# Optimization experiments

Hardware: AMD Instinct MI355X
Metric: run time of the kernel (lower is better)

Reference implementation:

```python
import jax, jax.numpy as jnp
import numpy as np

N, D, T = 4096, 512, 4096
TEMPERATURE = 0.07
MARGIN = 0.5
CONT_WEIGHT = 1.0
TRIP_WEIGHT = 0.3
EPS = 1e-8        # eps in the log / denominator (matches torch code)
PD_EPS = 1e-6     # F.pairwise_distance default eps added to the difference


def setup_inputs() -> dict:
    key = jax.random.key(0)
    k1, k2, k3 = jax.random.split(key, 3)
    embeddings = jax.random.normal(k1, (N, D), dtype=jnp.float32)
    labels = jax.random.randint(k2, (N,), 0, 256)            # ~16 positives per place
    triplets = jax.random.randint(k3, (T, 3), 0, N)          # (anchor, pos, neg) indices
    return {"embeddings": embeddings, "labels": labels, "triplets": triplets}


def reference(embeddings, labels, triplets):
    # ---- MultiPositiveContrastiveLoss ----
    # F.cosine_similarity normalizes each row with eps=1e-8 on the norm.
    norms = jnp.linalg.norm(embeddings, axis=1, keepdims=True)
    n_emb = embeddings / jnp.maximum(norms, EPS)
    sim = (n_emb @ n_emb.T) / TEMPERATURE                    # [N, N]

    pos_mask = (labels[:, None] == labels[None, :]).astype(embeddings.dtype)
    pos_mask = pos_mask * (1.0 - jnp.eye(sim.shape[0], dtype=embeddings.dtype))

    exp_sim = jnp.exp(sim)
    pos_sum = (exp_sim * pos_mask).sum(axis=1)
    total_sum = exp_sim.sum(axis=1)
    loss = -jnp.log(pos_sum / (total_sum + EPS) + EPS)

    valid = pos_mask.sum(axis=1) > 0
    cnt = valid.sum()
    cont_loss = jnp.where(
        cnt > 0,
        jnp.where(valid, loss, 0.0).sum() / jnp.maximum(cnt, 1).astype(loss.dtype),
        jnp.zeros((), loss.dtype),
    )

    # ---- TripletLoss, vectorized over all triplets (replaces Python loop) ----
    a = embeddings[triplets[:, 0]]   # [T, D]
    p = embeddings[triplets[:, 1]]
    ng = embeddings[triplets[:, 2]]
    pos_dist = jnp.linalg.norm(a - p + PD_EPS, axis=1)
    neg_dist = jnp.linalg.norm(a - ng + PD_EPS, axis=1)
    trip_loss = jnp.maximum(pos_dist - neg_dist + MARGIN, 0.0).mean()

    total = CONT_WEIGHT * cont_loss + TRIP_WEIGHT * trip_loss
    return (total, cont_loss, trip_loss)
```

## Files before the change

### kernel.cpp

```cpp
#include <hip/hip_runtime.h>

#define NN 4096
#define DD 512
#define TT 4096

typedef __bf16 bf16x8 __attribute__((ext_vector_type(8)));
typedef float f32x4 __attribute__((ext_vector_type(4)));

constexpr float INV_TEMP = 1.0f / 0.07f;

#define AS1(p) ((__attribute__((address_space(1))) const void*)(p))
#define AS3(p) ((__attribute__((address_space(3))) void*)(p))

__global__ __launch_bounds__(256) void k_normalize(const float* __restrict__ emb,
                                                   __bf16* __restrict__ nemb) {
    int wave = threadIdx.x >> 6, lane = threadIdx.x & 63;
    int row = blockIdx.x * 4 + wave;
    const float4* src = (const float4*)(emb + (size_t)row * DD);
    float4 x0 = src[lane * 2 + 0];
    float4 x1 = src[lane * 2 + 1];
    float ss = x0.x * x0.x + x0.y * x0.y + x0.z * x0.z + x0.w * x0.w +
               x1.x * x1.x + x1.y * x1.y + x1.z * x1.z + x1.w * x1.w;
    #pragma unroll
    for (int m = 1; m < 64; m <<= 1) ss += __shfl_xor(ss, m, 64);
    float inv = 1.0f / fmaxf(sqrtf(ss), 1e-8f);
    bf16x8 v;
    v[0] = (__bf16)(x0.x * inv); v[1] = (__bf16)(x0.y * inv);
    v[2] = (__bf16)(x0.z * inv); v[3] = (__bf16)(x0.w * inv);
    v[4] = (__bf16)(x1.x * inv); v[5] = (__bf16)(x1.y * inv);
    v[6] = (__bf16)(x1.z * inv); v[7] = (__bf16)(x1.w * inv);
    *(bf16x8*)(nemb + (size_t)row * DD + lane * 8) = v;
}

__global__ __launch_bounds__(256) void k_contrast(const __bf16* __restrict__ nemb,
                                                  const int* __restrict__ labels,
                                                  float* __restrict__ posP,
                                                  float* __restrict__ totP,
                                                  float* __restrict__ cntP) {
    __shared__ __attribute__((aligned(16))) __bf16 aSm[128 * 32];
    __shared__ __attribute__((aligned(16))) __bf16 bSm[128 * 32];
    __shared__ int rlab[128];
    __shared__ int clab[128];

    int tid = threadIdx.x;
    int lane = tid & 63, wave = tid >> 6;
    int wr = wave >> 1, wc = wave & 1;
    int l15 = lane & 15, quad = lane >> 4;
    int rowblk = blockIdx.y, colblk = blockIdx.x;
    int row0 = rowblk * 128, col0 = colblk * 128;

    if (tid < 128) rlab[tid] = labels[row0 + tid];
    else           clab[tid - 128] = labels[col0 + tid - 128];

    f32x4 acc[4][4];
    #pragma unroll
    for (int r = 0; r < 4; ++r)
        #pragma unroll
        for (int c = 0; c < 4; ++c) {
            f32x4 z = {0.0f, 0.0f, 0.0f, 0.0f};
            acc[r][c] = z;
        }

    const __bf16* gA = nemb + (size_t)(row0 + (tid >> 2)) * DD + (tid & 3) * 8;
    const __bf16* gB = nemb + (size_t)(col0 + (tid >> 2)) * DD + (tid & 3) * 8;

    for (int kt = 0; kt < 16; ++kt) {
        int kb = kt * 32;
        __syncthreads();
        __builtin_amdgcn_global_load_lds(AS1(gA + kb),                     AS3(aSm + tid * 8),         16, 0, 0);
        __builtin_amdgcn_global_load_lds(AS1(gA + (size_t)64 * DD + kb),   AS3(aSm + (tid + 256) * 8), 16, 0, 0);
        __builtin_amdgcn_global_load_lds(AS1(gB + kb),                     AS3(bSm + tid * 8),         16, 0, 0);
        __builtin_amdgcn_global_load_lds(AS1(gB + (size_t)64 * DD + kb),   AS3(bSm + (tid + 256) * 8), 16, 0, 0);
        __syncthreads();

        bf16x8 af[4], bfr[4];
        #pragma unroll
        for (int r = 0; r < 4; ++r)
            af[r] = *(const bf16x8*)(aSm + (wr * 64 + r * 16 + l15) * 32 + quad * 8);
        #pragma unroll
        for (int c = 0; c < 4; ++c)
            bfr[c] = *(const bf16x8*)(bSm + (wc * 64 + c * 16 + l15) * 32 + quad * 8);
        #pragma unroll
        for (int r = 0; r < 4; ++r)
            #pragma unroll
            for (int c = 0; c < 4; ++c)
                acc[r][c] = __builtin_amdgcn_mfma_f32_16x16x32_bf16(af[r], bfr[c], acc[r][c], 0, 0, 0);
    }

    int cl[4];
    #pragma unroll
    for (int c = 0; c < 4; ++c) cl[c] = clab[wc * 64 + c * 16 + l15];

    #pragma unroll
    for (int r = 0; r < 4; ++r) {
        float tv[4] = {0, 0, 0, 0}, pv[4] = {0, 0, 0, 0}, cv[4] = {0, 0, 0, 0};
        int gibase = row0 + wr * 64 + r * 16 + quad * 4;
        int rl[4];
        #pragma unroll
        for (int v = 0; v < 4; ++v) rl[v] = rlab[wr * 64 + r * 16 + quad * 4 + v];
        #pragma unroll
        for (int c = 0; c < 4; ++c) {
            int gj = col0 + wc * 64 + c * 16 + l15;
            #pragma unroll
            for (int v = 0; v < 4; ++v) {
                float e = __expf(acc[r][c][v] * INV_TEMP);
                tv[v] += e;
                bool match = (rl[v] == cl[c]) && ((gibase + v) != gj);
                pv[v] += match ? e : 0.0f;
                cv[v] += match ? 1.0f : 0.0f;
            }
        }
        #pragma unroll
        for (int m = 1; m < 16; m <<= 1) {
            #pragma unroll
            for (int v = 0; v < 4; ++v) {
                tv[v] += __shfl_xor(tv[v], m, 64);
                pv[v] += __shfl_xor(pv[v], m, 64);
                cv[v] += __shfl_xor(cv[v], m, 64);
            }
        }
        if (l15 == 0) {
            #pragma unroll
            for (int v = 0; v < 4; ++v) {
                int gr = gibase + v;
                int oidx = gr * 64 + colblk * 2 + wc;
                posP[oidx] = pv[v];
                totP[oidx] = tv[v];
                cntP[oidx] = cv[v];
            }
        }
    }
}

__global__ __launch_bounds__(256) void k_triplet(const float* __restrict__ emb,
                                                 const int* __restrict__ trip,
                                                 float* __restrict__ tl) {
    int wave = threadIdx.x >> 6, lane = threadIdx.x & 63;
    int t = blockIdx.x * 4 + wave;
    int ia = trip[t * 3 + 0], ip = trip[t * 3 + 1], ig = trip[t * 3 + 2];
    const float4* pa = (const float4*)(emb + (size_t)ia * DD);
    const float4* pp = (const float4*)(emb + (size_t)ip * DD);
    const float4* pn = (const float4*)(emb + (size_t)ig * DD);
    float d1 = 0.0f, d2 = 0.0f;
    #pragma unroll
    for (int j = 0; j < 2; ++j) {
        float4 a = pa[lane * 2 + j];
        float4 p = pp[lane * 2 + j];
        float4 n = pn[lane * 2 + j];
        float dx;
        dx = a.x - p.x + 1e-6f; d1 += dx * dx;
        dx = a.y - p.y + 1e-6f; d1 += dx * dx;
        dx = a.z - p.z + 1e-6f; d1 += dx * dx;
        dx = a.w - p.w + 1e-6f; d1 += dx * dx;
        dx = a.x - n.x + 1e-6f; d2 += dx * dx;
        dx = a.y - n.y + 1e-6f; d2 += dx * dx;
        dx = a.z - n.z + 1e-6f; d2 += dx * dx;
        dx = a.w - n.w + 1e-6f; d2 += dx * dx;
    }
    #pragma unroll
    for (int m = 1; m < 64; m <<= 1) {
        d1 += __shfl_xor(d1, m, 64);
        d2 += __shfl_xor(d2, m, 64);
    }
    if (lane == 0) tl[t] = fmaxf(sqrtf(d1) - sqrtf(d2) + 0.5f, 0.0f);
}

__global__ __launch_bounds__(256) void k_rowloss(const float* __restrict__ posP,
                                                 const float* __restrict__ totP,
                                                 const float* __restrict__ cntP,
                                                 float* __restrict__ rloss,
                                                 float* __restrict__ rvalid) {
    int wave = threadIdx.x >> 6, lane = threadIdx.x & 63;
    int row = blockIdx.x * 4 + wave;
    float p = posP[row * 64 + lane];
    float t = totP[row * 64 + lane];
    float c = cntP[row * 64 + lane];
    #pragma unroll
    for (int m = 1; m < 64; m <<= 1) {
        p += __shfl_xor(p, m, 64);
        t += __shfl_xor(t, m, 64);
        c += __shfl_xor(c, m, 64);
    }
    if (lane == 0) {
        float loss = -logf(p / (t + 1e-8f) + 1e-8f);
        bool valid = c > 0.0f;
        rloss[row] = valid ? loss : 0.0f;
        rvalid[row] = valid ? 1.0f : 0.0f;
    }
}

__global__ __launch_bounds__(256) void k_final(const float* __restrict__ rloss,
                                               const float* __restrict__ rvalid,
                                               const float* __restrict__ tl,
                                               float* __restrict__ out) {
    int tid = threadIdx.x;
    float sl = 0.0f, sv = 0.0f, st = 0.0f;
    for (int i = tid; i < NN; i += 256) {
        sl += rloss[i];
        sv += rvalid[i];
        st += tl[i];
    }
    #pragma unroll
    for (int m = 1; m < 64; m <<= 1) {
        sl += __shfl_xor(sl, m, 64);
        sv += __shfl_xor(sv, m, 64);
        st += __shfl_xor(st, m, 64);
    }
    __shared__ float red[3][4];
    int lane = tid & 63, wave = tid >> 6;
    if (lane == 0) { red[0][wave] = sl; red[1][wave] = sv; red[2][wave] = st; }
    __syncthreads();
    if (tid == 0) {
        float SL = red[0][0] + red[0][1] + red[0][2] + red[0][3];
        float SV = red[1][0] + red[1][1] + red[1][2] + red[1][3];
        float ST = red[2][0] + red[2][1] + red[2][2] + red[2][3];
        float cont = (SV > 0.0f) ? (SL / SV) : 0.0f;
        float trip = ST * (1.0f / (float)TT);
        out[0] = cont + 0.3f * trip;
        out[1] = cont;
        out[2] = trip;
    }
}

extern "C" void kernel_launch(void* const* d_in, const int* in_sizes, int n_in,
                              void* d_out, int out_size, void* d_ws, size_t ws_size,
                              hipStream_t stream) {
    const float* emb = (const float*)d_in[0];
    const int* labels = (const int*)d_in[1];
    const int* trips = (const int*)d_in[2];
    float* out = (float*)d_out;
    char* ws = (char*)d_ws;

    __bf16* nemb  = (__bf16*)(ws);
    float* posP   = (float*)(ws + 4194304);
    float* totP   = (float*)(ws + 5242880);
    float* cntP   = (float*)(ws + 6291456);
    float* rloss  = (float*)(ws + 7340032);
    float* rvalid = (float*)(ws + 7356416);
    float* tl     = (float*)(ws + 7372800);

    k_normalize<<<NN / 4, 256, 0, stream>>>(emb, nemb);
    k_contrast<<<dim3(32, 32), 256, 0, stream>>>(nemb, labels, posP, totP, cntP);
    k_triplet<<<TT / 4, 256, 0, stream>>>(emb, trips, tl);
    k_rowloss<<<NN / 4, 256, 0, stream>>>(posP, totP, cntP, rloss, rvalid);
    k_final<<<1, 256, 0, stream>>>(rloss, rvalid, tl, out);
}
```

Measured before the change: 111.9 us.

## Exploit Gram matrix symmetry with triangular tiles and fuse normalize with triplet kernel

The contrastive kernel now computes only upper-triangular 128x128 block pairs of the symmetric similarity matrix. Each block is split into two 64-row halves, and each off-diagonal tile emits both row and column partial sums, so the N^2 MFMA and exp work is roughly halved. The normalize and triplet kernels are merged into one launch to save a launch and let them overlap. The cost is a smaller per-block tile with less operand reuse, extra column-direction reductions and stores, and a wider partial-sum buffer for the row-loss kernel to read.

```diff
diff --git a/kernel.cpp b/kernel.cpp
--- a/kernel.cpp
+++ b/kernel.cpp
@@ -12,24 +12,56 @@
 #define AS1(p) ((__attribute__((address_space(1))) const void*)(p))
 #define AS3(p) ((__attribute__((address_space(3))) void*)(p))
 
-__global__ __launch_bounds__(256) void k_normalize(const float* __restrict__ emb,
-                                                   __bf16* __restrict__ nemb) {
+__global__ __launch_bounds__(256) void k_normtrip(const float* __restrict__ emb,
+                                                  const int* __restrict__ trip,
+                                                  __bf16* __restrict__ nemb,
+                                                  float* __restrict__ tl) {
     int wave = threadIdx.x >> 6, lane = threadIdx.x & 63;
-    int row = blockIdx.x * 4 + wave;
-    const float4* src = (const float4*)(emb + (size_t)row * DD);
-    float4 x0 = src[lane * 2 + 0];
-    float4 x1 = src[lane * 2 + 1];
-    float ss = x0.x * x0.x + x0.y * x0.y + x0.z * x0.z + x0.w * x0.w +
-               x1.x * x1.x + x1.y * x1.y + x1.z * x1.z + x1.w * x1.w;
-    #pragma unroll
-    for (int m = 1; m < 64; m <<= 1) ss += __shfl_xor(ss, m, 64);
-    float inv = 1.0f / fmaxf(sqrtf(ss), 1e-8f);
-    bf16x8 v;
-    v[0] = (__bf16)(x0.x * inv); v[1] = (__bf16)(x0.y * inv);
-    v[2] = (__bf16)(x0.z * inv); v[3] = (__bf16)(x0.w * inv);
-    v[4] = (__bf16)(x1.x * inv); v[5] = (__bf16)(x1.y * inv);
-    v[6] = (__bf16)(x1.z * inv); v[7] = (__bf16)(x1.w * inv);
-    *(bf16x8*)(nemb + (size_t)row * DD + lane * 8) = v;
+    if (blockIdx.x < NN / 4) {
+        int row = blockIdx.x * 4 + wave;
+        const float4* src = (const float4*)(emb + (size_t)row * DD);
+        float4 x0 = src[lane * 2 + 0];
+        float4 x1 = src[lane * 2 + 1];
+        float ss = x0.x * x0.x + x0.y * x0.y + x0.z * x0.z + x0.w * x0.w +
+                   x1.x * x1.x + x1.y * x1.y + x1.z * x1.z + x1.w * x1.w;
+        #pragma unroll
+        for (int m = 1; m < 64; m <<= 1) ss += __shfl_xor(ss, m, 64);
+        float inv = 1.0f / fmaxf(sqrtf(ss), 1e-8f);
+        bf16x8 v;
+        v[0] = (__bf16)(x0.x * inv); v[1] = (__bf16)(x0.y * inv);
+        v[2] = (__bf16)(x0.z * inv); v[3] = (__bf16)(x0.w * inv);
+        v[4] = (__bf16)(x1.x * inv); v[5] = (__bf16)(x1.y * inv);
+        v[6] = (__bf16)(x1.z * inv); v[7] = (__bf16)(x1.w * inv);
+        *(bf16x8*)(nemb + (size_t)row * DD + lane * 8) = v;
+    } else {
+        int t = (blockIdx.x - NN / 4) * 4 + wave;
+        int ia = trip[t * 3 + 0], ip = trip[t * 3 + 1], ig = trip[t * 3 + 2];
+        const float4* pa = (const float4*)(emb + (size_t)ia * DD);
+        const float4* pp = (const float4*)(emb + (size_t)ip * DD);
+        const float4* pn = (const float4*)(emb + (size_t)ig * DD);
+        float d1 = 0.0f, d2 = 0.0f;
+        #pragma unroll
+        for (int j = 0; j < 2; ++j) {
+            float4 a = pa[lane * 2 + j];
+            float4 p = pp[lane * 2 + j];
+            float4 n = pn[lane * 2 + j];
+            float dx;
+            dx = a.x - p.x + 1e-6f; d1 += dx * dx;
+            dx = a.y - p.y + 1e-6f; d1 += dx * dx;
+            dx = a.z - p.z + 1e-6f; d1 += dx * dx;
+            dx = a.w - p.w + 1e-6f; d1 += dx * dx;
+            dx = a.x - n.x + 1e-6f; d2 += dx * dx;
+            dx = a.y - n.y + 1e-6f; d2 += dx * dx;
+            dx = a.z - n.z + 1e-6f; d2 += dx * dx;
+            dx = a.w - n.w + 1e-6f; d2 += dx * dx;
+        }
+        #pragma unroll
+        for (int m = 1; m < 64; m <<= 1) {
+            d1 += __shfl_xor(d1, m, 64);
+            d2 += __shfl_xor(d2, m, 64);
+        }
+        if (lane == 0) tl[t] = fmaxf(sqrtf(d1) - sqrtf(d2) + 0.5f, 0.0f);
+    }
 }
 
 __global__ __launch_bounds__(256) void k_contrast(const __bf16* __restrict__ nemb,
@@ -37,26 +69,34 @@
                                                   float* __restrict__ posP,
                                                   float* __restrict__ totP,
                                                   float* __restrict__ cntP) {
-    __shared__ __attribute__((aligned(16))) __bf16 aSm[128 * 32];
+    __shared__ __attribute__((aligned(16))) __bf16 aSm[64 * 32];
     __shared__ __attribute__((aligned(16))) __bf16 bSm[128 * 32];
-    __shared__ int rlab[128];
+    __shared__ int rlab[64];
     __shared__ int clab[128];
 
     int tid = threadIdx.x;
     int lane = tid & 63, wave = tid >> 6;
-    int wr = wave >> 1, wc = wave & 1;
+    int wc = wave;
     int l15 = lane & 15, quad = lane >> 4;
-    int rowblk = blockIdx.y, colblk = blockIdx.x;
-    int row0 = rowblk * 128, col0 = colblk * 128;
-
-    if (tid < 128) rlab[tid] = labels[row0 + tid];
-    else           clab[tid - 128] = labels[col0 + tid - 128];
-
-    f32x4 acc[4][4];
+
+    int idx = blockIdx.y;
+    int half = blockIdx.x;
+    int cb = (int)((sqrtf(8.0f * (float)idx + 1.0f) - 1.0f) * 0.5f);
+    while ((cb + 1) * (cb + 2) / 2 <= idx) ++cb;
+    while (cb * (cb + 1) / 2 > idx) --cb;
+    int rb = idx - cb * (cb + 1) / 2;
+    int row0 = rb * 128 + half * 64;
+    int col0 = cb * 128;
+    bool offd = (rb != cb);
+
+    if (tid < 64)       rlab[tid] = labels[row0 + tid];
+    else if (tid < 192) clab[tid - 64] = labels[col0 + tid - 64];
+
+    f32x4 acc[4][2];
     #pragma unroll
     for (int r = 0; r < 4; ++r)
         #pragma unroll
-        for (int c = 0; c < 4; ++c) {
+        for (int c = 0; c < 2; ++c) {
             f32x4 z = {0.0f, 0.0f, 0.0f, 0.0f};
             acc[r][c] = z;
         }
@@ -67,47 +107,50 @@
     for (int kt = 0; kt < 16; ++kt) {
         int kb = kt * 32;
         __syncthreads();
-        __builtin_amdgcn_global_load_lds(AS1(gA + kb),                     AS3(aSm + tid * 8),         16, 0, 0);
-        __builtin_amdgcn_global_load_lds(AS1(gA + (size_t)64 * DD + kb),   AS3(aSm + (tid + 256) * 8), 16, 0, 0);
-        __builtin_amdgcn_global_load_lds(AS1(gB + kb),                     AS3(bSm + tid * 8),         16, 0, 0);
-        __builtin_amdgcn_global_load_lds(AS1(gB + (size_t)64 * DD + kb),   AS3(bSm + (tid + 256) * 8), 16, 0, 0);
+        __builtin_amdgcn_global_load_lds(AS1(gA + kb),                   AS3(aSm + tid * 8),         16, 0, 0);
+        __builtin_amdgcn_global_load_lds(AS1(gB + kb),                   AS3(bSm + tid * 8),         16, 0, 0);
+        __builtin_amdgcn_global_load_lds(AS1(gB + (size_t)64 * DD + kb), AS3(bSm + (tid + 256) * 8), 16, 0, 0);
         __syncthreads();
 
-        bf16x8 af[4], bfr[4];
+        bf16x8 af[4], bfr[2];
         #pragma unroll
         for (int r = 0; r < 4; ++r)
-            af[r] = *(const bf16x8*)(aSm + (wr * 64 + r * 16 + l15) * 32 + quad * 8);
-        #pragma unroll
-        for (int c = 0; c < 4; ++c)
-            bfr[c] = *(const bf16x8*)(bSm + (wc * 64 + c * 16 + l15) * 32 + quad * 8);
+            af[r] = *(const bf16x8*)(aSm + (r * 16 + l15) * 32 + quad * 8);
+        #pragma unroll
+        for (int c = 0; c < 2; ++c)
+            bfr[c] = *(const bf16x8*)(bSm + (wc * 32 + c * 16 + l15) * 32 + quad * 8);
         #pragma unroll
         for (int r = 0; r < 4; ++r)
             #pragma unroll
-            for (int c = 0; c < 4; ++c)
+            for (int c = 0; c < 2; ++c)
                 acc[r][c] = __builtin_amdgcn_mfma_f32_16x16x32_bf16(af[r], bfr[c], acc[r][c], 0, 0, 0);
     }
 
-    int cl[4];
-    #pragma unroll
-    for (int c = 0; c < 4; ++c) cl[c] = clab[wc * 64 + c * 16 + l15];
+    int cl[2];
+    #pragma unroll
+    for (int c = 0; c < 2; ++c) cl[c] = clab[wc * 32 + c * 16 + l15];
+
+    float tT[2] = {0, 0}, pT[2] = {0, 0}, cT[2] = {0, 0};
+    int rslotbase = (cb - rb) * 4 + wc;
 
     #pragma unroll
     for (int r = 0; r < 4; ++r) {
         float tv[4] = {0, 0, 0, 0}, pv[4] = {0, 0, 0, 0}, cv[4] = {0, 0, 0, 0};
-        int gibase = row0 + wr * 64 + r * 16 + quad * 4;
+        int gibase = row0 + r * 16 + quad * 4;
         int rl[4];
         #pragma unroll
-        for (int v = 0; v < 4; ++v) rl[v] = rlab[wr * 64 + r * 16 + quad * 4 + v];
-        #pragma unroll
-        for (int c = 0; c < 4; ++c) {
-            int gj = col0 + wc * 64 + c * 16 + l15;
+        for (int v = 0; v < 4; ++v) rl[v] = rlab[r * 16 + quad * 4 + v];
+        #pragma unroll
+        for (int c = 0; c < 2; ++c) {
+            int gj = col0 + wc * 32 + c * 16 + l15;
             #pragma unroll
             for (int v = 0; v < 4; ++v) {
                 float e = __expf(acc[r][c][v] * INV_TEMP);
-                tv[v] += e;
                 bool match = (rl[v] == cl[c]) && ((gibase + v) != gj);
-                pv[v] += match ? e : 0.0f;
-                cv[v] += match ? 1.0f : 0.0f;
+                float me = match ? e : 0.0f;
+                float mc = match ? 1.0f : 0.0f;
+                tv[v] += e;  pv[v] += me;  cv[v] += mc;
+                tT[c] += e;  pT[c] += me;  cT[c] += mc;
             }
         }
         #pragma unroll
@@ -123,46 +166,36 @@
             #pragma unroll
             for (int v = 0; v < 4; ++v) {
                 int gr = gibase + v;
-                int oidx = gr * 64 + colblk * 2 + wc;
+                int oidx = gr * 128 + rslotbase;
                 posP[oidx] = pv[v];
                 totP[oidx] = tv[v];
                 cntP[oidx] = cv[v];
             }
         }
     }
-}
-
-__global__ __launch_bounds__(256) void k_triplet(const float* __restrict__ emb,
-                                                 const int* __restrict__ trip,
-                                                 float* __restrict__ tl) {
-    int wave = threadIdx.x >> 6, lane = threadIdx.x & 63;
-    int t = blockIdx.x * 4 + wave;
-    int ia = trip[t * 3 + 0], ip = trip[t * 3 + 1], ig = trip[t * 3 + 2];
-    const float4* pa = (const float4*)(emb + (size_t)ia * DD);
-    const float4* pp = (const float4*)(emb + (size_t)ip * DD);
-    const float4* pn = (const float4*)(emb + (size_t)ig * DD);
-    float d1 = 0.0f, d2 = 0.0f;
-    #pragma unroll
-    for (int j = 0; j < 2; ++j) {
-        float4 a = pa[lane * 2 + j];
-        float4 p = pp[lane * 2 + j];
-        float4 n = pn[lane * 2 + j];
-        float dx;
-        dx = a.x - p.x + 1e-6f; d1 += dx * dx;
-        dx = a.y - p.y + 1e-6f; d1 += dx * dx;
-        dx = a.z - p.z + 1e-6f; d1 += dx * dx;
-        dx = a.w - p.w + 1e-6f; d1 += dx * dx;
-        dx = a.x - n.x + 1e-6f; d2 += dx * dx;
-        dx = a.y - n.y + 1e-6f; d2 += dx * dx;
-        dx = a.z - n.z + 1e-6f; d2 += dx * dx;
-        dx = a.w - n.w + 1e-6f; d2 += dx * dx;
-    }
-    #pragma unroll
-    for (int m = 1; m < 64; m <<= 1) {
-        d1 += __shfl_xor(d1, m, 64);
-        d2 += __shfl_xor(d2, m, 64);
-    }
-    if (lane == 0) tl[t] = fmaxf(sqrtf(d1) - sqrtf(d2) + 0.5f, 0.0f);
+
+    if (offd) {
+        #pragma unroll
+        for (int m = 16; m < 64; m <<= 1) {
+            #pragma unroll
+            for (int c = 0; c < 2; ++c) {
+                tT[c] += __shfl_xor(tT[c], m, 64);
+                pT[c] += __shfl_xor(pT[c], m, 64);
+                cT[c] += __shfl_xor(cT[c], m, 64);
+            }
+        }
+        if (quad == 0) {
+            int mslot = 4 * (32 - cb) + rb * 2 + half;
+            #pragma unroll
+            for (int c = 0; c < 2; ++c) {
+                int gj = col0 + wc * 32 + c * 16 + l15;
+                int oidx = gj * 128 + mslot;
+                posP[oidx] = pT[c];
+                totP[oidx] = tT[c];
+                cntP[oidx] = cT[c];
+            }
+        }
+    }
 }
 
 __global__ __launch_bounds__(256) void k_rowloss(const float* __restrict__ posP,
@@ -172,9 +205,15 @@
                                                  float* __restrict__ rvalid) {
     int wave = threadIdx.x >> 6, lane = threadIdx.x & 63;
     int row = blockIdx.x * 4 + wave;
-    float p = posP[row * 64 + lane];
-    float t = totP[row * 64 + lane];
-    float c = cntP[row * 64 + lane];
+    int used = 128 - 2 * (row >> 7);
+    float p = posP[row * 128 + lane];
+    float t = totP[row * 128 + lane];
+    float c = cntP[row * 128 + lane];
+    if (64 + lane < used) {
+        p += posP[row * 128 + 64 + lane];
+        t += totP[row * 128 + 64 + lane];
+        c += cntP[row * 128 + 64 + lane];
+    }
     #pragma unroll
     for (int m = 1; m < 64; m <<= 1) {
         p += __shfl_xor(p, m, 64);
@@ -233,15 +272,14 @@
 
     __bf16* nemb  = (__bf16*)(ws);
     float* posP   = (float*)(ws + 4194304);
-    float* totP   = (float*)(ws + 5242880);
-    float* cntP   = (float*)(ws + 6291456);
-    float* rloss  = (float*)(ws + 7340032);
-    float* rvalid = (float*)(ws + 7356416);
-    float* tl     = (float*)(ws + 7372800);
-
-    k_normalize<<<NN / 4, 256, 0, stream>>>(emb, nemb);
-    k_contrast<<<dim3(32, 32), 256, 0, stream>>>(nemb, labels, posP, totP, cntP);
-    k_triplet<<<TT / 4, 256, 0, stream>>>(emb, trips, tl);
+    float* totP   = (float*)(ws + 6291456);
+    float* cntP   = (float*)(ws + 8388608);
+    float* rloss  = (float*)(ws + 10485760);
+    float* rvalid = (float*)(ws + 10502144);
+    float* tl     = (float*)(ws + 10518528);
+
+    k_normtrip<<<NN / 4 + TT / 4, 256, 0, stream>>>(emb, trips, nemb, tl);
+    k_contrast<<<dim3(2, 528), 256, 0, stream>>>(nemb, labels, posP, totP, cntP);
     k_rowloss<<<NN / 4, 256, 0, stream>>>(posP, totP, cntP, rloss, rvalid);
     k_final<<<1, 256, 0, stream>>>(rloss, rvalid, tl, out);
 }
```

Measured after the change: 112.8 us. Within noise of the previous version (+0.8%).
